# Performance work log

Hardware: AMD Instinct MI355X
Metric: run time of the kernel (lower is better)

The kernel has to match this reference:

```python
import jax, jax.numpy as jnp
import numpy as np

B, C, L, K = 8, 128, 32768, 129  # batch, seq_len (channels), samples, filter length


def setup_inputs() -> dict:
    key = jax.random.key(0)
    k0, k1, k2, k3 = jax.random.split(key, 4)
    return {
        "x": jax.random.normal(k0, (B, C, L), dtype=jnp.float32),
        "weights_mag": jnp.ones((C, 1), dtype=jnp.float32),
        "weights_angle": jax.random.uniform(k1, (C, 1), dtype=jnp.float32),
        "kernel_real": jax.random.normal(k2, (K,), dtype=jnp.float32),
        "kernel_imag": jax.random.normal(k3, (K,), dtype=jnp.float32),
    }


def _matched_filter(x, kr, ki):
    # PyTorch F.conv1d is cross-correlation; mf_coeffs = conj(kernel) repeated per
    # channel (groups = C), so every channel is correlated with the SAME conj kernel.
    # Input is real (x.to(complex64) has zero imag), so:
    #   out = corr(x, conj(k)) = corr(x, kr) - 1j * corr(x, ki)
    b, c, l = x.shape
    kk = kr.shape[0]
    pad = kk // 2
    w = jnp.stack([kr, -ki])[:, None, :]  # [2, 1, K]: real and imag of conj kernel
    y = jax.lax.conv_general_dilated(
        x.reshape(b * c, 1, l), w,
        window_strides=(1,), padding=[(pad, pad)],
        dimension_numbers=("NCH", "OIH", "NCH"),
    )  # [B*C, 2, L]
    yr = y[:, 0].reshape(b, c, l)
    yi = y[:, 1].reshape(b, c, l)
    return yr + 1j * yi  # complex64


def reference(x, weights_mag, weights_angle, kernel_real, kernel_imag):
    batch = x.shape[0]
    y = _matched_filter(x, kernel_real, kernel_imag)          # [B, C, L] complex64
    phase = jnp.arctan(weights_angle)                          # [C, 1]
    norm_mag = batch * jax.nn.softmax(weights_mag, axis=0)     # [C, 1]
    scale = (norm_mag.astype(jnp.complex64) * jnp.exp(-1j * phase))  # [C, 1] complex
    return scale * y
```

## Files before the change

kernel.cpp:

```cpp
#include <hip/hip_runtime.h>
#include <hip/hip_bf16.h>
#include <math.h>

constexpr int Bc = 8, Cc = 128, Lc = 32768, Kc = 129, PAD = 64;

constexpr int MLEN = 256;
constexpr int T    = 16;
constexpr int NSEG = Lc / (MLEN * T);
constexpr int WPB  = 4;
constexpr int THREADS = 64 * WPB;
constexpr int LASTCW  = Lc / MLEN - 1;

typedef __attribute__((ext_vector_type(8))) short short8;
typedef __attribute__((ext_vector_type(4))) float floatx4;

#define WAITVM(N) do { asm volatile("s_waitcnt vmcnt(" #N ")" ::: "memory"); \
                       __builtin_amdgcn_sched_barrier(0); } while (0)
#define WAITLG()  do { asm volatile("s_waitcnt lgkmcnt(0)" ::: "memory"); \
                       __builtin_amdgcn_sched_barrier(0); } while (0)

__device__ __forceinline__ unsigned short f2bf(float f) {
    return __builtin_bit_cast(unsigned short, __float2bfloat16(f));
}

__device__ __forceinline__ short8 cvt8(const float4& a, const float4& b) {
    __hip_bfloat162 p0 = __float22bfloat162_rn(make_float2(a.x, a.y));
    __hip_bfloat162 p1 = __float22bfloat162_rn(make_float2(a.z, a.w));
    __hip_bfloat162 p2 = __float22bfloat162_rn(make_float2(b.x, b.y));
    __hip_bfloat162 p3 = __float22bfloat162_rn(make_float2(b.z, b.w));
    ushort2 u0, u1, u2, u3;
    __builtin_memcpy(&u0, &p0, 4);
    __builtin_memcpy(&u1, &p1, 4);
    __builtin_memcpy(&u2, &p2, 4);
    __builtin_memcpy(&u3, &p3, 4);
    short8 r;
    r[0] = (short)u0.x; r[1] = (short)u0.y;
    r[2] = (short)u1.x; r[3] = (short)u1.y;
    r[4] = (short)u2.x; r[5] = (short)u2.y;
    r[6] = (short)u3.x; r[7] = (short)u3.y;
    return r;
}

__device__ __forceinline__ void gload_lds16(const float* g, void* l) {
    auto gp = (const __attribute__((address_space(1))) void*)g;
    auto lp = (__attribute__((address_space(3))) void*)l;
    __builtin_amdgcn_global_load_lds(gp, lp, 16, 0, 0);
}

__global__ void scale_kernel(const float* __restrict__ wm,
                             const float* __restrict__ wa,
                             float* __restrict__ ws, int C, float batchf) {
    int c = threadIdx.x;
    if (c >= C) return;
    float m = -1e30f;
    for (int i = 0; i < C; ++i) m = fmaxf(m, wm[i]);
    float s = 0.f;
    for (int i = 0; i < C; ++i) s += expf(wm[i] - m);
    float nm = batchf * expf(wm[c] - m) / s;
    float a = wa[c];
    float inv = rsqrtf(1.f + a * a);
    ws[2 * c]     = nm * inv;
    ws[2 * c + 1] = nm * a * inv;
}

__global__ __launch_bounds__(THREADS, 5)
void mf_kernel(const float* __restrict__ x,
               const float* __restrict__ kr,
               const float* __restrict__ ki,
               const float* __restrict__ sc_ss,
               float* __restrict__ out, int interleaved) {
    __shared__ __align__(16) float          lf[WPB][2][512];
    __shared__ __align__(16) unsigned short lb[WPB][2][512];

    const int seg = blockIdx.x;
    const int rg  = blockIdx.y;
    const int tid = threadIdx.x;
    const int lane= tid & 63;
    const int wv  = tid >> 6;
    const int fh  = lane >> 4;
    const int fn  = lane & 15;

    const int row = rg * WPB + wv;
    const int cw0 = seg * T;

    short8 br[5], bi[5];
    #pragma unroll
    for (int d = 0; d < 5; ++d) {
        #pragma unroll
        for (int e = 0; e < 8; ++e) {
            int idx = 32 * d + 8 * fh + e - fn;
            bool ok = (idx >= 0) && (idx < Kc);
            br[d][e] = (short)f2bf(ok ? kr[idx] : 0.f);
            bi[d][e] = (short)f2bf(ok ? ki[idx] : 0.f);
        }
    }

    const int ch = row & (Cc - 1);
    const float scv = sc_ss[2 * ch];
    const float ssv = sc_ss[2 * ch + 1];

    const float* __restrict__ xrow = x + (size_t)row * Lc;

    auto DMA = [&](int cw, int buf) {
        const float* g = xrow + (cw * MLEN - PAD) + 4 * lane;
        char* l = (char*)&lf[wv][buf][0];
        gload_lds16(g, l);
        gload_lds16(g + 256, l + 1024);
    };

    auto TILE = [&](int cw, int buf) {
        const unsigned short* ab = &lb[wv][buf][0];
        short8 a[5];
        #pragma unroll
        for (int d = 0; d < 5; ++d)
            a[d] = *reinterpret_cast<const short8*>(ab + 16 * fn + 8 * fh + 32 * d);
        WAITLG();
        floatx4 cr = {0.f, 0.f, 0.f, 0.f};
        floatx4 ci = {0.f, 0.f, 0.f, 0.f};
        #pragma unroll
        for (int d = 0; d < 5; ++d) {
            cr = __builtin_amdgcn_mfma_f32_16x16x32_bf16(a[d], br[d], cr, 0, 0, 0);
            ci = __builtin_amdgcn_mfma_f32_16x16x32_bf16(a[d], bi[d], ci, 0, 0, 0);
        }
        if (!interleaved) {
            float* op = out + (size_t)row * Lc + cw * MLEN + 64 * fh + fn;
            #pragma unroll
            for (int r = 0; r < 4; ++r)
                op[16 * r] = scv * cr[r] - ssv * ci[r];
        } else {
            float2* op = reinterpret_cast<float2*>(out) +
                         ((size_t)row * Lc + cw * MLEN + 64 * fh + fn);
            #pragma unroll
            for (int r = 0; r < 4; ++r)
                op[16 * r] = make_float2(scv * cr[r] - ssv * ci[r],
                                         -scv * ci[r] - ssv * cr[r]);
        }
    };

    if (cw0 != 0) DMA(cw0, 0);
    DMA(cw0 + 1, 1);

    #pragma unroll
    for (int c = 0; c < T; ++c) {
        const int cw  = cw0 + c;
        const int buf = c & 1;
        const bool edge = (cw == 0) || (cw == LASTCW);

        if (edge) {
            const int g0 = cw * MLEN - PAD + 8 * lane;
            float vv[8];
            #pragma unroll
            for (int jj = 0; jj < 8; ++jj) {
                const int g = g0 + jj;
                vv[jj] = (g >= 0 && g < Lc) ? xrow[g] : 0.f;
            }
            if (c + 2 < T) DMA(cw + 2, buf);
            float4 va = make_float4(vv[0], vv[1], vv[2], vv[3]);
            float4 vb = make_float4(vv[4], vv[5], vv[6], vv[7]);
            short8 h = cvt8(va, vb);
            *reinterpret_cast<short8*>(&lb[wv][buf][8 * lane]) = h;
            WAITLG();
            TILE(cw, buf);
        } else {
            if (c == 0)          WAITVM(2);
            else if (c == 1)     WAITVM(6);
            else if (c >= T - 2) WAITVM(8);
            else                 WAITVM(10);

            const floatx4* lp = reinterpret_cast<const floatx4*>(&lf[wv][buf][0]);
            floatx4 va4 = lp[2 * lane];
            floatx4 vb4 = lp[2 * lane + 1];
            WAITLG();
            if (c + 2 < T && (cw + 2) != LASTCW) DMA(cw + 2, buf);
            float4 va = make_float4(va4[0], va4[1], va4[2], va4[3]);
            float4 vb = make_float4(vb4[0], vb4[1], vb4[2], vb4[3]);
            short8 h = cvt8(va, vb);
            *reinterpret_cast<short8*>(&lb[wv][buf][8 * lane]) = h;
            WAITLG();
            TILE(cw, buf);
        }
    }
}

extern "C" void kernel_launch(void* const* d_in, const int* in_sizes, int n_in,
                              void* d_out, int out_size, void* d_ws, size_t ws_size,
                              hipStream_t stream) {
    const float* x  = (const float*)d_in[0];
    const float* wm = (const float*)d_in[1];
    const float* wa = (const float*)d_in[2];
    const float* kr = (const float*)d_in[3];
    const float* ki = (const float*)d_in[4];
    float* out = (float*)d_out;
    float* ws  = (float*)d_ws;

    const int C = in_sizes[1];
    const long long N = (long long)Bc * Cc * Lc;
    const int interleaved = (out_size == 2 * N) ? 1 : 0;

    hipLaunchKernelGGL(scale_kernel, dim3(1), dim3(C), 0, stream,
                       wm, wa, ws, C, (float)Bc);

    dim3 grid(NSEG, (Bc * Cc) / WPB);
    hipLaunchKernelGGL(mf_kernel, grid, dim3(THREADS), 0, stream,
                       x, kr, ki, ws, out, interleaved);
}
```

Measured before the change: 70.47 us.

## Load MFMA operands directly from global into registers, dropping LDS staging

Removes the LDS round trip, in which x was DMA'd into LDS as fp32, converted to bf16, and written back to LDS before being read as MFMA A-fragments. Each lane now loads the overlapping fp32 window it needs straight into registers with float4 loads, double-buffered across iterations. Edge tiles are handled by clamping addresses and zeroing the out-of-range elements. This reads each input value about five times from global/L2 instead of once and needs many more VGPRs, so the launch-bounds occupancy hint drops from 5 to 3.

New measurement: 215.5 us. 206% more time.

```diff
diff --git a/kernel.cpp b/kernel.cpp
--- a/kernel.cpp
+++ b/kernel.cpp
@@ -15,8 +15,6 @@
 typedef __attribute__((ext_vector_type(4))) float floatx4;
 
 #define WAITVM(N) do { asm volatile("s_waitcnt vmcnt(" #N ")" ::: "memory"); \
-                       __builtin_amdgcn_sched_barrier(0); } while (0)
-#define WAITLG()  do { asm volatile("s_waitcnt lgkmcnt(0)" ::: "memory"); \
                        __builtin_amdgcn_sched_barrier(0); } while (0)
 
 __device__ __forceinline__ unsigned short f2bf(float f) {
@@ -41,12 +39,6 @@
     return r;
 }
 
-__device__ __forceinline__ void gload_lds16(const float* g, void* l) {
-    auto gp = (const __attribute__((address_space(1))) void*)g;
-    auto lp = (__attribute__((address_space(3))) void*)l;
-    __builtin_amdgcn_global_load_lds(gp, lp, 16, 0, 0);
-}
-
 __global__ void scale_kernel(const float* __restrict__ wm,
                              const float* __restrict__ wa,
                              float* __restrict__ ws, int C, float batchf) {
@@ -63,15 +55,12 @@
     ws[2 * c + 1] = nm * a * inv;
 }
 
-__global__ __launch_bounds__(THREADS, 5)
+__global__ __launch_bounds__(THREADS, 3)
 void mf_kernel(const float* __restrict__ x,
                const float* __restrict__ kr,
                const float* __restrict__ ki,
                const float* __restrict__ sc_ss,
                float* __restrict__ out, int interleaved) {
-    __shared__ __align__(16) float          lf[WPB][2][512];
-    __shared__ __align__(16) unsigned short lb[WPB][2][512];
-
     const int seg = blockIdx.x;
     const int rg  = blockIdx.y;
     const int tid = threadIdx.x;
@@ -79,6 +68,7 @@
     const int wv  = tid >> 6;
     const int fh  = lane >> 4;
     const int fn  = lane & 15;
+    const int loff= 16 * fn + 8 * fh;
 
     const int row = rg * WPB + wv;
     const int cw0 = seg * T;
@@ -101,20 +91,61 @@
 
     const float* __restrict__ xrow = x + (size_t)row * Lc;
 
-    auto DMA = [&](int cw, int buf) {
-        const float* g = xrow + (cw * MLEN - PAD) + 4 * lane;
-        char* l = (char*)&lf[wv][buf][0];
-        gload_lds16(g, l);
-        gload_lds16(g + 256, l + 1024);
+    float4 F[2][10];
+
+    auto ISSUE = [&](int cw, int buf) {
+        const int g0 = cw * MLEN - PAD + loff;
+        if (cw == 0 || cw == LASTCW) {
+            #pragma unroll
+            for (int d = 0; d < 5; ++d) {
+                int ga = min(max(g0 + 32 * d, 0), Lc - 4);
+                int gb = min(max(g0 + 32 * d + 4, 0), Lc - 4);
+                F[buf][2 * d]     = *reinterpret_cast<const float4*>(xrow + ga);
+                F[buf][2 * d + 1] = *reinterpret_cast<const float4*>(xrow + gb);
+            }
+        } else {
+            #pragma unroll
+            for (int d = 0; d < 5; ++d) {
+                F[buf][2 * d]     = *reinterpret_cast<const float4*>(xrow + g0 + 32 * d);
+                F[buf][2 * d + 1] = *reinterpret_cast<const float4*>(xrow + g0 + 32 * d + 4);
+            }
+        }
     };
 
-    auto TILE = [&](int cw, int buf) {
-        const unsigned short* ab = &lb[wv][buf][0];
+    ISSUE(cw0, 0);
+    ISSUE(cw0 + 1, 1);
+
+    #pragma unroll
+    for (int c = 0; c < T; ++c) {
+        const int cw  = cw0 + c;
+        const int buf = c & 1;
+
+        if (c == 0)          WAITVM(10);
+        else if (c == 1)     WAITVM(14);
+        else if (c == T - 1) WAITVM(8);
+        else                 WAITVM(18);
+
         short8 a[5];
         #pragma unroll
         for (int d = 0; d < 5; ++d)
-            a[d] = *reinterpret_cast<const short8*>(ab + 16 * fn + 8 * fh + 32 * d);
-        WAITLG();
+            a[d] = cvt8(F[buf][2 * d], F[buf][2 * d + 1]);
+
+        if (cw == 0) {
+            #pragma unroll
+            for (int d = 0; d < 2; ++d)
+                #pragma unroll
+                for (int e = 0; e < 8; ++e)
+                    if (loff + 32 * d + e < 64) a[d][e] = 0;
+        } else if (cw == LASTCW) {
+            #pragma unroll
+            for (int d = 2; d < 5; ++d)
+                #pragma unroll
+                for (int e = 0; e < 8; ++e)
+                    if (loff + 32 * d + e >= 320) a[d][e] = 0;
+        }
+
+        if (c + 2 < T) ISSUE(cw0 + c + 2, buf);
+
         floatx4 cr = {0.f, 0.f, 0.f, 0.f};
         floatx4 ci = {0.f, 0.f, 0.f, 0.f};
         #pragma unroll
@@ -122,6 +153,7 @@
             cr = __builtin_amdgcn_mfma_f32_16x16x32_bf16(a[d], br[d], cr, 0, 0, 0);
             ci = __builtin_amdgcn_mfma_f32_16x16x32_bf16(a[d], bi[d], ci, 0, 0, 0);
         }
+
         if (!interleaved) {
             float* op = out + (size_t)row * Lc + cw * MLEN + 64 * fh + fn;
             #pragma unroll
@@ -134,50 +166,6 @@
             for (int r = 0; r < 4; ++r)
                 op[16 * r] = make_float2(scv * cr[r] - ssv * ci[r],
                                          -scv * ci[r] - ssv * cr[r]);
-        }
-    };
-
-    if (cw0 != 0) DMA(cw0, 0);
-    DMA(cw0 + 1, 1);
-
-    #pragma unroll
-    for (int c = 0; c < T; ++c) {
-        const int cw  = cw0 + c;
-        const int buf = c & 1;
-        const bool edge = (cw == 0) || (cw == LASTCW);
-
-        if (edge) {
-            const int g0 = cw * MLEN - PAD + 8 * lane;
-            float vv[8];
-            #pragma unroll
-            for (int jj = 0; jj < 8; ++jj) {
-                const int g = g0 + jj;
-                vv[jj] = (g >= 0 && g < Lc) ? xrow[g] : 0.f;
-            }
-            if (c + 2 < T) DMA(cw + 2, buf);
-            float4 va = make_float4(vv[0], vv[1], vv[2], vv[3]);
-            float4 vb = make_float4(vv[4], vv[5], vv[6], vv[7]);
-            short8 h = cvt8(va, vb);
-            *reinterpret_cast<short8*>(&lb[wv][buf][8 * lane]) = h;
-            WAITLG();
-            TILE(cw, buf);
-        } else {
-            if (c == 0)          WAITVM(2);
-            else if (c == 1)     WAITVM(6);
-            else if (c >= T - 2) WAITVM(8);
-            else                 WAITVM(10);
-
-            const floatx4* lp = reinterpret_cast<const floatx4*>(&lf[wv][buf][0]);
-            floatx4 va4 = lp[2 * lane];
-            floatx4 vb4 = lp[2 * lane + 1];
-            WAITLG();
-            if (c + 2 < T && (cw + 2) != LASTCW) DMA(cw + 2, buf);
-            float4 va = make_float4(va4[0], va4[1], va4[2], va4[3]);
-            float4 vb = make_float4(vb4[0], vb4[1], vb4[2], vb4[3]);
-            short8 h = cvt8(va, vb);
-            *reinterpret_cast<short8*>(&lb[wv][buf][8 * lane]) = h;
-            WAITLG();
-            TILE(cw, buf);
         }
     }
 }
```
